# Optimization experiments

Measured on AMD Instinct MI355X. Metric: run time of the kernel, lower is better.

Reference implementation:

```python
import jax, jax.numpy as jnp
import numpy as np
from jax import lax

# FPN anchor layout: 800x800 image, 3 anchors/loc, strides 4,8,16,32,64
LEVEL_ANCHORS = [120000, 30000, 7500, 1875, 507]
PRE_NMS_TOP_N = 1000   # per level (test mode)
POST_NMS_TOP_N = 1000
NMS_THRESH = 0.7
MIN_SIZE = 1e-3


def setup_inputs() -> dict:
    key = jax.random.key(0)
    k1, k2, k3, k4 = jax.random.split(key, 4)
    A = sum(LEVEL_ANCHORS)
    bs = 2
    predicts = jax.random.normal(k1, (bs, A, 4), jnp.float32) * 0.1
    objectness = jax.random.normal(k2, (bs, A, 1), jnp.float32)
    cxy = jax.random.uniform(k3, (A, 2), jnp.float32, 0.0, 800.0)
    wh = jax.random.uniform(k4, (A, 2), jnp.float32, 16.0, 128.0)
    anchors = jnp.concatenate([cxy - 0.5 * wh, cxy + 0.5 * wh], axis=-1)
    valid_size = jnp.full((bs, 2), 800.0, jnp.float32)  # (w, h) per image
    return {"predicts": predicts, "objectness": objectness,
            "anchors": anchors, "valid_size": valid_size}


def _decode(predicts, anchors):
    # BoxCoder.decoder with weights [1,1,1,1]
    awh = anchors[:, 2:] - anchors[:, :2]          # [A,2]
    axy = anchors[:, :2] + 0.5 * awh               # [A,2]
    xy = axy + predicts[..., :2] * awh             # [bs,A,2] center
    wh = jnp.exp(predicts[..., 2:]) * awh          # [bs,A,2]
    x1y1 = xy - 0.5 * wh
    return jnp.concatenate([x1y1, x1y1 + wh], axis=-1)  # [bs,A,4]


def _per_level_topk_idx(scores):
    # scores: [bs, A] -> concat of per-level top-k indices (global anchor ids)
    idx_list, offset = [], 0
    for n in LEVEL_ANCHORS:
        k = min(PRE_NMS_TOP_N, n)
        _, top = lax.top_k(scores[:, offset:offset + n], k)
        idx_list.append(top + offset)
        offset += n
    return jnp.concatenate(idx_list, axis=1)  # [bs, K]


def _nms_keep(boxes, valid, thresh):
    # boxes sorted by score desc; returns boolean keep mask (sequential NMS)
    x1, y1, x2, y2 = boxes[:, 0], boxes[:, 1], boxes[:, 2], boxes[:, 3]
    area = (x2 - x1) * (y2 - y1)
    xx1 = jnp.maximum(x1[:, None], x1[None, :])
    yy1 = jnp.maximum(y1[:, None], y1[None, :])
    xx2 = jnp.minimum(x2[:, None], x2[None, :])
    yy2 = jnp.minimum(y2[:, None], y2[None, :])
    inter = jnp.maximum(xx2 - xx1, 0.0) * jnp.maximum(yy2 - yy1, 0.0)
    iou = inter / (area[:, None] + area[None, :] - inter + 1e-9)
    sup = iou > thresh                                   # [N,N]
    N = boxes.shape[0]
    ar = jnp.arange(N)

    def body(i, keep):
        suppressed = jnp.any((ar < i) & keep & sup[i])
        return keep.at[i].set(keep[i] & ~suppressed)

    return lax.fori_loop(0, N, body, valid)


def _filter_image(boxes, scores, lvls, wh):
    # boxes [K,4], scores [K], lvls [K] int, wh [2]=(w,h)
    w, h = wh[0], wh[1]
    x1 = jnp.clip(boxes[:, 0], 0.0, w)
    y1 = jnp.clip(boxes[:, 1], 0.0, h)
    x2 = jnp.clip(boxes[:, 2], 0.0, w)
    y2 = jnp.clip(boxes[:, 3], 0.0, h)
    boxes = jnp.stack([x1, y1, x2, y2], axis=-1)
    valid = (x2 - x1 > MIN_SIZE) & (y2 - y1 > MIN_SIZE)
    s = jnp.where(valid, scores, -jnp.inf)
    order = jnp.argsort(-s)
    boxes, s, lvls, valid = boxes[order], s[order], lvls[order], valid[order]
    # batched_nms: offset each level into a disjoint coordinate range
    max_coord = lax.stop_gradient(jnp.max(boxes)) + 1.0
    off = lvls.astype(boxes.dtype) * max_coord
    keep = _nms_keep(lax.stop_gradient(boxes) + off[:, None], valid, NMS_THRESH)
    # take first POST_NMS_TOP_N kept (boxes are score-sorted)
    rank = jnp.cumsum(keep) - 1
    slot = jnp.where(keep & (rank < POST_NMS_TOP_N), rank, POST_NMS_TOP_N)
    out_b = jnp.zeros((POST_NMS_TOP_N + 1, 4), boxes.dtype).at[slot].set(boxes)[:POST_NMS_TOP_N]
    out_s = jnp.zeros((POST_NMS_TOP_N + 1,), s.dtype).at[slot].set(
        jnp.where(keep, s, 0.0))[:POST_NMS_TOP_N]
    return out_b, out_s


def reference(predicts, objectness, anchors, valid_size):
    bs = predicts.shape[0]
    proposals = _decode(predicts, anchors)            # [bs,A,4]
    scores = objectness[..., 0]                       # [bs,A]
    idx = _per_level_topk_idx(scores)                 # [bs,K]
    bidx = jnp.arange(bs)[:, None]
    boxes = proposals[bidx, idx]                      # [bs,K,4]
    sc = scores[bidx, idx]                            # [bs,K]
    levels_all = jnp.concatenate(
        [jnp.full((n,), i, jnp.int32) for i, n in enumerate(LEVEL_ANCHORS)])
    lvl = levels_all[idx]                             # [bs,K]
    final_boxes, final_scores = jax.vmap(_filter_image)(boxes, sc, lvl, valid_size)
    return final_boxes, final_scores
```

## Files before the change

### kernel.cpp

```cpp
#include <hip/hip_runtime.h>

typedef unsigned int u32;
typedef unsigned long long u64;

#define A_TOT    159882
#define BS       2
#define KTOP     1000
#define CAND_CAP 4096
#define HB       4096
#define ABLK     4096
#define NBH      40
#define NBLK     (BS * NBH)

static const size_t HIST12_OFF   = 0;
static const size_t CCNT_OFF     = 131072;
static const size_t MAXC_OFF     = 131104;
static const size_t NV_OFF       = 131112;
static const size_t CUTV_OFF     = 131152;
static const size_t BAR_OFF      = 131184;
static const size_t CHUNKANY_OFF = 131264;
static const size_t KEEPS_OFF    = 132544;
static const size_t ZERO_END     = 133824;
static const size_t CAND_OFF     = 133824;
static const size_t LKEY2_OFF    = 395968;
static const size_t LBOX_OFF     = 477888;
static const size_t LSC_OFF      = 641728;
static const size_t RANK_OFF     = 682688;
static const size_t MASK_OFF     = 723648;

__device__ __forceinline__ int level_of(int a) {
  if (a < 120000) return 0;
  if (a < 150000) return 1;
  if (a < 157500) return 2;
  if (a < 159375) return 3;
  return 4;
}

__device__ __forceinline__ u32 dkey(float s) {
  u32 b = __float_as_uint(s);
  return (b & 0x80000000u) ? b : (~b & 0x7FFFFFFFu);
}
__device__ __forceinline__ float dkey_inv(u32 d) {
  u32 b = (d & 0x80000000u) ? d : (~d & 0x7FFFFFFFu);
  return __uint_as_float(b);
}

__device__ __forceinline__ u32 ld_agent_u32(const u32* p) {
  return __hip_atomic_load(p, __ATOMIC_RELAXED, __HIP_MEMORY_SCOPE_AGENT);
}
__device__ __forceinline__ u64 ld_agent_u64(const u64* p) {
  return __hip_atomic_load(p, __ATOMIC_RELAXED, __HIP_MEMORY_SCOPE_AGENT);
}
__device__ __forceinline__ void st_agent_u32(u32* p, u32 v) {
  __hip_atomic_store(p, v, __ATOMIC_RELAXED, __HIP_MEMORY_SCOPE_AGENT);
}
__device__ __forceinline__ void st_agent_u64(u64* p, u64 v) {
  __hip_atomic_store(p, v, __ATOMIC_RELAXED, __HIP_MEMORY_SCOPE_AGENT);
}

__device__ __forceinline__ void gb_arrive(u32* cnt) {
  __syncthreads();
  if (threadIdx.x == 0)
    __hip_atomic_fetch_add(cnt, 1u, __ATOMIC_ACQ_REL, __HIP_MEMORY_SCOPE_AGENT);
}
__device__ __forceinline__ void gb_wait(u32* cnt, u32 nblk) {
  if (threadIdx.x == 0) {
    while (__hip_atomic_load(cnt, __ATOMIC_ACQUIRE, __HIP_MEMORY_SCOPE_AGENT) < nblk)
      __builtin_amdgcn_s_sleep(2);
  }
  __syncthreads();
}

__device__ __forceinline__ void decode_clip(const float* __restrict__ pred,
                                            const float* __restrict__ anch,
                                            const float* __restrict__ vs,
                                            int b, int a,
                                            float& x1c, float& y1c, float& x2c, float& y2c,
                                            bool& valid) {
  const float* pp = pred + ((size_t)b * A_TOT + (size_t)a) * 4;
  const float* aa = anch + (size_t)a * 4;
  float ax1 = aa[0], ay1 = aa[1], ax2 = aa[2], ay2 = aa[3];
  float px = pp[0], py = pp[1], pw = pp[2], ph = pp[3];
  float aw  = __fsub_rn(ax2, ax1);
  float ah  = __fsub_rn(ay2, ay1);
  float acx = __fadd_rn(ax1, __fmul_rn(0.5f, aw));
  float acy = __fadd_rn(ay1, __fmul_rn(0.5f, ah));
  float cx  = __fadd_rn(acx, __fmul_rn(px, aw));
  float cy  = __fadd_rn(acy, __fmul_rn(py, ah));
  float w   = __fmul_rn(expf(pw), aw);
  float h   = __fmul_rn(expf(ph), ah);
  float x1  = __fsub_rn(cx, __fmul_rn(0.5f, w));
  float y1  = __fsub_rn(cy, __fmul_rn(0.5f, h));
  float x2  = __fadd_rn(x1, w);
  float y2  = __fadd_rn(y1, h);
  float Wv = vs[b * 2 + 0], Hv = vs[b * 2 + 1];
  x1c = fminf(fmaxf(x1, 0.0f), Wv);
  y1c = fminf(fmaxf(y1, 0.0f), Hv);
  x2c = fminf(fmaxf(x2, 0.0f), Wv);
  y2c = fminf(fmaxf(y2, 0.0f), Hv);
  valid = (__fsub_rn(x2c, x1c) > 0.001f) && (__fsub_rn(y2c, y1c) > 0.001f);
}

__device__ __forceinline__ void bitonic_u64(u64* arr, int N, int t, int nt) {
  for (int k = 2; k <= N; k <<= 1) {
    for (int j = k >> 1; j > 0; j >>= 1) {
      __syncthreads();
      for (int i = t; i < N; i += nt) {
        int ixj = i ^ j;
        if (ixj > i) {
          u64 x = arr[i], y = arr[ixj];
          bool up = ((i & k) == 0);
          if (up ? (x > y) : (x < y)) { arr[i] = y; arr[ixj] = x; }
        }
      }
    }
  }
  __syncthreads();
}

__device__ __forceinline__ u64 shfl_xor_u64(u64 x, int lanemask) {
  u32 lo = (u32)x, hi = (u32)(x >> 32);
  lo = (u32)__shfl_xor((int)lo, lanemask);
  hi = (u32)__shfl_xor((int)hi, lanemask);
  return ((u64)hi << 32) | (u64)lo;
}

__device__ __forceinline__ u64* regsort2048x(u64 v[2], int tid, u64* bufA, u64* bufB) {
  u64* bufs[2] = {bufA, bufB};
  int cur = 0;
  for (int k = 2; k <= 2048; k <<= 1) {
    for (int j = k >> 1; j > 0; j >>= 1) {
      if (j == 1) {
        bool up = (((2 * tid) & k) == 0);
        u64 a = v[0], b2 = v[1];
        bool sw = up ? (a > b2) : (a < b2);
        if (sw) { v[0] = b2; v[1] = a; }
      } else if (j <= 64) {
        int dl = j >> 1;
        bool up = (((2 * tid) & k) == 0);
        bool low = ((tid & dl) == 0);
        bool keepmin = (low == up);
#pragma unroll
        for (int e = 0; e < 2; ++e) {
          u64 o = shfl_xor_u64(v[e], dl);
          v[e] = keepmin ? (v[e] < o ? v[e] : o) : (v[e] > o ? v[e] : o);
        }
      } else {
        u64* B = bufs[cur]; cur ^= 1;
        B[2 * tid] = v[0]; B[2 * tid + 1] = v[1];
        __syncthreads();
#pragma unroll
        for (int e = 0; e < 2; ++e) {
          int i = 2 * tid + e, p = i ^ j;
          u64 o = B[p];
          bool up = ((i & k) == 0);
          bool keepmin = ((i < p) == up);
          v[e] = keepmin ? (v[e] < o ? v[e] : o) : (v[e] > o ? v[e] : o);
        }
      }
    }
  }
  u64* B = bufs[cur];
  B[2 * tid] = v[0]; B[2 * tid + 1] = v[1];
  __syncthreads();
  return B;
}

__global__ __launch_bounds__(1024)
void k_selsort(const float* __restrict__ pred, const float* __restrict__ obj,
               const float* __restrict__ anch, const float* __restrict__ vs,
               char* __restrict__ ws) {
  __shared__ __align__(16) char smem[82048];
  __shared__ u32 lcnt[2], gbase[2], cutL[2];
  u32* h  = (u32*)smem;
  u32* dk = (u32*)(smem + 32768);
  int tid = threadIdx.x, lane = tid & 63;
  int bid = blockIdx.x;
  int b = bid / NBH, loc = bid % NBH;
  int start = loc * ABLK;
  int l0 = level_of(start);
  bool active = (l0 < 4);
  int nseg = 0;
  u32* barp = (u32*)(ws + BAR_OFF);

  if (active) {
    int lend = level_of(min(start + ABLK - 1, A_TOT - 1));
    nseg = ((l0 + 1 <= lend) && (l0 + 1 < 4)) ? 2 : 1;
    for (int i = tid; i < 2 * HB; i += 1024) h[i] = 0u;
    __syncthreads();
#pragma unroll
    for (int it = 0; it < 4; ++it) {
      int a = start + it * 1024 + tid;
      u32 d = 0;
      if (a < A_TOT) {
        d = dkey(obj[(size_t)b * A_TOT + a]);
        int l = level_of(a);
        if (l < 4) atomicAdd(&h[(u32)(l - l0) * HB + (d >> 20)], 1u);
      }
      dk[it * 1024 + tid] = d;
    }
    __syncthreads();
    for (int s = 0; s < nseg; ++s) {
      u32* gh = (u32*)(ws + HIST12_OFF) + (size_t)(b * 4 + l0 + s) * HB;
      for (int i = tid; i < HB; i += 1024) {
        u32 v = h[s * HB + i];
        if (v) atomicAdd(&gh[i], v);
      }
    }
  }
  gb_arrive(barp + 0); gb_wait(barp + 0, NBLK);

  if (bid < 8) {
    u32* scanS = (u32*)smem;
    const u32* gh = (const u32*)(ws + HIST12_OFF) + (size_t)bid * HB;
    u32 vals[16]; u32 acc = 0;
    if (tid < 256) {
      for (int q = 0; q < 16; ++q) { vals[q] = ld_agent_u32(&gh[tid * 16 + q]); acc += vals[q]; }
      scanS[tid] = acc;
    }
    __syncthreads();
    for (int d = 1; d < 256; d <<= 1) {
      u32 x = (tid < 256 && tid >= d) ? scanS[tid - d] : 0u;
      __syncthreads();
      if (tid < 256) scanS[tid] += x;
      __syncthreads();
    }
    if (tid < 256) {
      u32 incl = scanS[tid], prev = incl - acc;
      if (prev < KTOP && incl >= KTOP) {
        u32 run = prev; int cb = HB - 1;
        for (int q = 0; q < 16; ++q) { run += vals[q]; if (run >= KTOP) { cb = tid * 16 + q; break; } }
        st_agent_u32((u32*)(ws + CUTV_OFF) + bid, (u32)cb);
      }
    }
  }
  gb_arrive(barp + 1); gb_wait(barp + 1, NBLK);

  if (active) {
    if (tid < 2) lcnt[tid] = 0;
    if (tid < nseg) cutL[tid] = ld_agent_u32((const u32*)(ws + CUTV_OFF) + b * 4 + l0 + tid);
    __syncthreads();
    u32 dv[4], slotv[4], passm = 0, sim = 0;
#pragma unroll
    for (int it = 0; it < 4; ++it) {
      int a = start + it * 1024 + tid;
      bool pass = false; u32 si = 0;
      u32 d = dk[it * 1024 + tid];
      if (a < A_TOT) {
        int l = level_of(a);
        if (l < 4) { si = (u32)(l - l0); pass = (d >> 20) <= cutL[si]; }
      }
      dv[it] = d;
      u64 mp = __ballot(pass);
      u64 m1 = __ballot(pass && si == 1);
      u64 m0 = mp & ~m1;
      u32 slot = 0;
      if (m0) {
        int ld = __builtin_ctzll(m0);
        u32 wb = 0;
        if (lane == ld) wb = atomicAdd(&lcnt[0], (u32)__popcll(m0));
        wb = __shfl(wb, ld);
        if (pass && si == 0) slot = wb + (u32)__popcll(m0 & ((1ull << lane) - 1ull));
      }
      if (m1) {
        int ld = __builtin_ctzll(m1);
        u32 wb = 0;
        if (lane == ld) wb = atomicAdd(&lcnt[1], (u32)__popcll(m1));
        wb = __shfl(wb, ld);
        if (pass && si == 1) slot = wb + (u32)__popcll(m1 & ((1ull << lane) - 1ull));
      }
      slotv[it] = slot;
      if (pass) { passm |= 1u << it; if (si) sim |= 1u << it; }
    }
    __syncthreads();
    if (tid < 2)
      gbase[tid] = lcnt[tid] ? atomicAdd((u32*)(ws + CCNT_OFF) + (b * 4 + l0 + tid), lcnt[tid]) : 0u;
    __syncthreads();
#pragma unroll
    for (int it = 0; it < 4; ++it) {
      if ((passm >> it) & 1u) {
        int a = start + it * 1024 + tid;
        u32 si = (sim >> it) & 1u;
        int seg = b * 4 + l0 + (int)si;
        u32 gslot = gbase[si] + slotv[it];
        if (gslot < CAND_CAP)
          st_agent_u64((u64*)(ws + CAND_OFF) + (size_t)seg * CAND_CAP + gslot,
                       ((u64)dv[it] << 32) | ((u64)(u32)a << 12) | (u64)gslot);
      }
    }
  }
  gb_arrive(barp + 2);
  if (bid >= 10) return;
  gb_wait(barp + 2, NBLK);

  u64*    bufAB  = (u64*)smem;
  float4* dboxS  = (float4*)(smem + 32768);
  float*  dscS   = (float*)(smem + 65536);
  u32*    validS = (u32*)(smem + 73728);
  u64*    cm     = (u64*)(smem + 81920);
  u64* bufA = bufAB; u64* bufB = bufAB + 2048;
  int wv = tid >> 6;
  int P = bid, l = P % 5;
  b = P / 5;
  int n;
  u64* S;
  if (l == 4) {
    n = 507;
    u64 v[2];
#pragma unroll
    for (int e = 0; e < 2; ++e) {
      int idx = 2 * tid + e;
      if (idx < 507) {
        int a = 159375 + idx;
        float sc = obj[(size_t)b * A_TOT + a];
        float x1, y1, x2, y2; bool valid;
        decode_clip(pred, anch, vs, b, a, x1, y1, x2, y2, valid);
        dboxS[idx] = make_float4(x1, y1, x2, y2);
        dscS[idx] = sc;
        validS[idx] = valid ? 1u : 0u;
        v[e] = ((u64)dkey(sc) << 32) | ((u64)(u32)a << 12) | (u64)idx;
      } else v[e] = ~0ull;
    }
    S = regsort2048x(v, tid, bufA, bufB);
  } else {
    n = KTOP;
    int seg = b * 4 + l;
    u32 cnt = min(ld_agent_u32((const u32*)(ws + CCNT_OFF) + seg), (u32)CAND_CAP);
    const u64* cand = (const u64*)(ws + CAND_OFF) + (size_t)seg * CAND_CAP;
    if (cnt <= 2048) {
      u64 v[2];
#pragma unroll
      for (int e = 0; e < 2; ++e) {
        int idx = 2 * tid + e;
        if (idx < (int)cnt) {
          u64 key = ld_agent_u64(&cand[idx]);
          int a = (int)((key >> 12) & 0x3FFFFu);
          float x1, y1, x2, y2; bool valid;
          decode_clip(pred, anch, vs, b, a, x1, y1, x2, y2, valid);
          dboxS[idx] = make_float4(x1, y1, x2, y2);
          dscS[idx] = dkey_inv((u32)(key >> 32));
          validS[idx] = valid ? 1u : 0u;
          v[e] = key;
        } else v[e] = ~0ull;
      }
      S = regsort2048x(v, tid, bufA, bufB);
    } else {
      int N = 2048; while (N < (int)cnt) N <<= 1;
      for (int i = tid; i < N; i += 1024)
        bufAB[i] = (i < (int)cnt) ? ld_agent_u64(&cand[i]) : ~0ull;
      bitonic_u64(bufAB, N, tid, 1024);
      for (int j = tid; j < KTOP; j += 1024) {
        u64 key = bufAB[j];
        int a = (int)((key >> 12) & 0x3FFFFu);
        float x1, y1, x2, y2; bool valid;
        decode_clip(pred, anch, vs, b, a, x1, y1, x2, y2, valid);
        dboxS[j] = make_float4(x1, y1, x2, y2);
        dscS[j] = dkey_inv((u32)(key >> 32));
        validS[j] = valid ? 1u : 0u;
        bufAB[j] = (key & ~0xFFFull) | (u64)j;
      }
      __syncthreads();
      S = bufAB;
    }
  }
  float m = 0.0f;
  for (int j = tid; j < n; j += 1024) {
    int slot = (int)(S[j] & 0xFFFull);
    float4 bx = dboxS[slot];
    m = fmaxf(m, fmaxf(fmaxf(bx.x, bx.y), fmaxf(bx.z, bx.w)));
  }
  for (int off = 32; off; off >>= 1) m = fmaxf(m, __shfl_xor(m, off));
  if (lane == 0) atomicMax((u32*)(ws + MAXC_OFF) + b, __float_as_uint(m));
  {
    int j = wv * 64 + lane;
    bool val = (j < n) && (validS[(int)(S[j] & 0xFFFull)] != 0u);
    u64 mask = __ballot(val);
    if (lane == 0) cm[wv] = mask;
    __syncthreads();
    int base = 0;
    for (int w2 = 0; w2 < wv; ++w2) base += __popcll(cm[w2]);
    if (val) {
      int r = base + __popcll(mask & ((1ull << lane) - 1ull));
      int slot = (int)(S[j] & 0xFFFull);
      ((u64*)(ws + LKEY2_OFF))[(size_t)P * 1024 + r] = S[j];
      ((float4*)(ws + LBOX_OFF))[(size_t)P * 1024 + r] = dboxS[slot];
      ((float*)(ws + LSC_OFF))[(size_t)P * 1024 + r] = dscS[slot];
    }
    if (tid == 0) {
      int tot = 0;
      for (int w2 = 0; w2 < 16; ++w2) tot += __popcll(cm[w2]);
      ((u32*)(ws + NV_OFF))[P] = (u32)tot;
    }
  }
}

__global__ __launch_bounds__(1024)
void k_nms(float* __restrict__ out, char* __restrict__ ws) {
  __shared__ __align__(16) char smem[130304];
  float4* boxS  = (float4*)smem;
  float*  areaS = (float*)(smem + 16384);
  u64*    maskL = (u64*)smem;
  u64* keepsF = (u64*)(smem + 128000);
  u64* kbF    = (u64*)(smem + 128640);
  u32* sbF    = (u32*)(smem + 129280);
  u32* pfxF   = (u32*)(smem + 129792);
  u32* nvsF   = (u32*)(smem + 130112);
  int tid = threadIdx.x, lane = tid & 63;
  int bid = blockIdx.x;
  int P = bid >> 4, rseg = bid & 15;
  int b = P / 5, l = P % 5;
  u32* barp = (u32*)(ws + BAR_OFF);
  int n = (int)((const u32*)(ws + NV_OFF))[P];
  int W = (n + 63) >> 6;
  {
    float M = __uint_as_float(((const u32*)(ws + MAXC_OFF))[b]);
    float off = __fmul_rn((float)l, __fadd_rn(M, 1.0f));
    const float4* lbox = (const float4*)(ws + LBOX_OFF) + (size_t)P * 1024;
    for (int i = tid; i < n; i += 1024) {
      float4 bx = lbox[i];
      bx.x = __fadd_rn(bx.x, off); bx.y = __fadd_rn(bx.y, off);
      bx.z = __fadd_rn(bx.z, off); bx.w = __fadd_rn(bx.w, off);
      boxS[i] = bx;
      areaS[i] = __fmul_rn(__fsub_rn(bx.z, bx.x), __fsub_rn(bx.w, bx.y));
    }
    if (tid < 64) {
      int e = rseg * 64 + tid;
      if (e < n) {
        const u64* lkey = (const u64*)(ws + LKEY2_OFF);
        const u32* nvp = (const u32*)(ws + NV_OFF);
        u64 key = lkey[(size_t)P * 1024 + e];
        const u64* base[4];
        int lo[4], hi[4], q2 = 0;
        for (int l2 = 0; l2 < 5; ++l2) {
          if (l2 == l) continue;
          base[q2] = lkey + (size_t)(b * 5 + l2) * 1024;
          lo[q2] = 0; hi[q2] = (int)nvp[b * 5 + l2];
          ++q2;
        }
        for (int step = 0; step < 11; ++step) {
#pragma unroll
          for (int q = 0; q < 4; ++q) {
            if (lo[q] < hi[q]) {
              int mid = (lo[q] + hi[q]) >> 1;
              u64 v = base[q][mid];
              if (v < key) lo[q] = mid + 1; else hi[q] = mid;
            }
          }
        }
        st_agent_u32((u32*)(ws + RANK_OFF) + (size_t)P * 1024 + e,
                     (u32)(e + lo[0] + lo[1] + lo[2] + lo[3]));
      }
    }
    __syncthreads();
    int i = rseg * 64 + (tid >> 4);
    int w = tid & 15;
    if (i < n && w < W && w >= rseg) {
      float4 bi = boxS[i];
      float ai = areaS[i];
      u64 word = 0;
      int j0 = w << 6;
      int jn = min(64, n - j0);
      if (jn == 64) {
#pragma unroll 4
        for (int t2 = 0; t2 < 64; ++t2) {
          int jj = (t2 + w) & 63;
          float4 bj = boxS[j0 + jj];
          float xx1 = fmaxf(bi.x, bj.x);
          float yy1 = fmaxf(bi.y, bj.y);
          float xx2 = fminf(bi.z, bj.z);
          float yy2 = fminf(bi.w, bj.w);
          float iw = fmaxf(__fsub_rn(xx2, xx1), 0.0f);
          float ih = fmaxf(__fsub_rn(yy2, yy1), 0.0f);
          float inter = __fmul_rn(iw, ih);
          float den = __fadd_rn(__fsub_rn(__fadd_rn(ai, areaS[j0 + jj]), inter), 1e-9f);
          float iou = __fdiv_rn(inter, den);
          if (iou > 0.7f) word |= (1ull << jj);
        }
      } else {
        for (int jj = 0; jj < jn; ++jj) {
          float4 bj = boxS[j0 + jj];
          float xx1 = fmaxf(bi.x, bj.x);
          float yy1 = fmaxf(bi.y, bj.y);
          float xx2 = fminf(bi.z, bj.z);
          float yy2 = fminf(bi.w, bj.w);
          float iw = fmaxf(__fsub_rn(xx2, xx1), 0.0f);
          float ih = fmaxf(__fsub_rn(yy2, yy1), 0.0f);
          float inter = __fmul_rn(iw, ih);
          float den = __fadd_rn(__fsub_rn(__fadd_rn(ai, areaS[j0 + jj]), inter), 1e-9f);
          float iou = __fdiv_rn(inter, den);
          if (iou > 0.7f) word |= (1ull << jj);
        }
      }
      if (w == rseg) word &= ~(1ull << (i & 63));
      st_agent_u64((u64*)(ws + MASK_OFF) + (size_t)P * 16000 + (size_t)i * W + w, word);
      if (word)
        atomicOr((u64*)(ws + CHUNKANY_OFF) + (size_t)P * 16 + (i >> 6), 1ull << (i & 63));
    }
  }
  gb_arrive(barp + 3);
  if (rseg != 0) return;
  gb_wait(barp + 3, 160);

  {
    const u64* maskg = (const u64*)(ws + MASK_OFF) + (size_t)P * 16000;
    int T = n * W;
    for (int t = tid; t < T; t += 1024) maskL[t] = ld_agent_u64(&maskg[t]);
    __syncthreads();
    if (tid < 64) {
      u64 ca = (lane < 16) ? ld_agent_u64((const u64*)(ws + CHUNKANY_OFF) + (size_t)P * 16 + lane)
                           : 0ull;
      u64 dpre[16];
#pragma unroll
      for (int c = 0; c < 16; ++c) {
        int row = (c << 6) + lane;
        dpre[c] = (c < W && row < n) ? maskL[(size_t)row * W + c] : 0ull;
      }
      u64 removed = 0ull, keepw = 0ull;
#pragma unroll
      for (int c = 0; c < 16; ++c) {
        if (c >= W) break;
        int rb = c << 6;
        int rows = min(64, n - rb);
        u64 rowsmask = (rows == 64) ? ~0ull : ((1ull << rows) - 1ull);
        u64 curw = __shfl(removed, c);
        u64 cand = ~curw & rowsmask;
        u64 ca_c = __shfl(ca, c);
        u64 keptbits;
        u64 anyrows = ca_c & cand;
        if (anyrows == 0ull) {
          keptbits = cand;
        } else {
          u64 diag = dpre[c];
          u64 diagnz = __ballot(diag != 0ull) & cand;
          if (diagnz == 0ull) {
            keptbits = cand;
          } else {
            u64 remw = curw | ~rowsmask;
            u64 kept = 0ull;
            int pos = 0;
            u64 work = diagnz;
            while (work) {
              int s = __builtin_ctzll(work); work &= work - 1;
              u64 range = (1ull << s) - (1ull << pos);
              kept |= ~remw & range;
              bool k = ((remw >> s) & 1ull) == 0ull;
              u64 dr = __shfl(diag, s);
              if (k) { kept |= 1ull << s; remw |= dr; }
              pos = s + 1;
            }
            u64 tail = (pos >= 64) ? 0ull : (~0ull << pos);
            kept |= ~remw & tail & rowsmask;
            keptbits = kept;
          }
          u64 todo = keptbits & ca_c;
          while (todo) {
            int r0 = __builtin_ctzll(todo); todo &= todo - 1;
            int r1 = -1, r2 = -1, r3 = -1;
            if (todo) { r1 = __builtin_ctzll(todo); todo &= todo - 1; }
            if (todo) { r2 = __builtin_ctzll(todo); todo &= todo - 1; }
            if (todo) { r3 = __builtin_ctzll(todo); todo &= todo - 1; }
            u64 v0 = 0, v1 = 0, v2 = 0, v3 = 0;
            if (lane < W) {
              v0 = maskL[(size_t)(rb + r0) * W + lane];
              if (r1 >= 0) v1 = maskL[(size_t)(rb + r1) * W + lane];
              if (r2 >= 0) v2 = maskL[(size_t)(rb + r2) * W + lane];
              if (r3 >= 0) v3 = maskL[(size_t)(rb + r3) * W + lane];
            }
            removed |= v0 | v1 | v2 | v3;
          }
        }
        if (lane == c) keepw |= keptbits;
      }
      if (lane < 16)
        st_agent_u64((u64*)(ws + KEEPS_OFF) + (size_t)P * 16 + lane, keepw);
    }
  }
  gb_arrive(barp + 4);
  if (l != 0) return;
  gb_wait(barp + 4, 10);

  for (int i = tid; i < 80; i += 1024) {
    keepsF[i] = ld_agent_u64((const u64*)(ws + KEEPS_OFF) + (size_t)b * 80 + i);
    kbF[i] = 0ull;
  }
  if (tid < 5) nvsF[tid] = ((const u32*)(ws + NV_OFF))[b * 5 + tid];
  for (int i = tid; i < 4000; i += 1024) out[(size_t)b * 4000 + i] = 0.0f;
  for (int i = tid; i < 1000; i += 1024) out[8000 + (size_t)b * 1000 + i] = 0.0f;
  __syncthreads();
  const u32* rank = (const u32*)(ws + RANK_OFF);
  for (int idx = tid; idx < 5120; idx += 1024) {
    int p = idx >> 10, i = idx & 1023;
    if (i < (int)nvsF[p] && ((keepsF[p * 16 + (i >> 6)] >> (i & 63)) & 1ull)) {
      u32 r = ld_agent_u32(&rank[(size_t)(b * 5 + p) * 1024 + i]);
      atomicOr(&kbF[r >> 6], 1ull << (r & 63));
    }
  }
  __syncthreads();
  if (tid < 128) sbF[tid] = (tid < 80) ? (u32)__popcll(kbF[tid]) : 0u;
  __syncthreads();
  for (int d = 1; d < 128; d <<= 1) {
    u32 x = (tid < 128 && tid >= d) ? sbF[tid - d] : 0u;
    __syncthreads();
    if (tid < 128) sbF[tid] += x;
    __syncthreads();
  }
  if (tid < 80) pfxF[tid] = sbF[tid] - (u32)__popcll(kbF[tid]);
  __syncthreads();
  for (int idx = tid; idx < 5120; idx += 1024) {
    int p = idx >> 10, i = idx & 1023;
    if (i < (int)nvsF[p] && ((keepsF[p * 16 + (i >> 6)] >> (i & 63)) & 1ull)) {
      int Pp = b * 5 + p;
      u32 r = ld_agent_u32(&rank[(size_t)Pp * 1024 + i]);
      u64 word = kbF[r >> 6];
      int slot = (int)pfxF[r >> 6] + __popcll(word & ((1ull << (r & 63)) - 1ull));
      if (slot < KTOP) {
        float4 bx = ((const float4*)(ws + LBOX_OFF))[(size_t)Pp * 1024 + i];
        float s = ((const float*)(ws + LSC_OFF))[(size_t)Pp * 1024 + i];
        float* ob = out + ((size_t)b * KTOP + slot) * 4;
        ob[0] = bx.x; ob[1] = bx.y; ob[2] = bx.z; ob[3] = bx.w;
        out[8000 + (size_t)b * KTOP + slot] = s;
      }
    }
  }
}

extern "C" void kernel_launch(void* const* d_in, const int* in_sizes, int n_in,
                              void* d_out, int out_size, void* d_ws, size_t ws_size,
                              hipStream_t stream) {
  const float* pred = (const float*)d_in[0];
  const float* obj  = (const float*)d_in[1];
  const float* anch = (const float*)d_in[2];
  const float* vs   = (const float*)d_in[3];
  float* out = (float*)d_out;
  char* ws = (char*)d_ws;
  (void)in_sizes; (void)n_in; (void)out_size; (void)ws_size;

  hipMemsetAsync(ws, 0, ZERO_END, stream);
  k_selsort<<<NBLK, 1024, 0, stream>>>(pred, obj, anch, vs, ws);
  k_nms    <<<160,  1024, 0, stream>>>(out, ws);
}
```

Before: 167.0 us.

## Fuse selection and NMS kernels into one with per-segment dataflow flags

Merges the two kernels into a single 160-block kernel. The grid-wide barriers are replaced by per-segment and per-image counters, so each stage waits only on its actual producers: histogram contributors, compaction, sort per image, mask rows per partition. Each block now computes its own cutoff scan, removing a barrier, and the cross-level binary search reads keys staged in shared memory. The cost is more shared memory per block, and correctness now depends on all 160 blocks being resident at once, since they spin-wait on each other.

Measured after the change: 196.6 us. 17.7% more time.

```diff
diff --git a/kernel.cpp b/kernel.cpp
--- a/kernel.cpp
+++ b/kernel.cpp
@@ -10,23 +10,25 @@
 #define HB       4096
 #define ABLK     4096
 #define NBH      40
-#define NBLK     (BS * NBH)
 
 static const size_t HIST12_OFF   = 0;
 static const size_t CCNT_OFF     = 131072;
 static const size_t MAXC_OFF     = 131104;
 static const size_t NV_OFF       = 131112;
-static const size_t CUTV_OFF     = 131152;
-static const size_t BAR_OFF      = 131184;
-static const size_t CHUNKANY_OFF = 131264;
-static const size_t KEEPS_OFF    = 132544;
-static const size_t ZERO_END     = 133824;
-static const size_t CAND_OFF     = 133824;
-static const size_t LKEY2_OFF    = 395968;
-static const size_t LBOX_OFF     = 477888;
-static const size_t LSC_OFF      = 641728;
-static const size_t RANK_OFF     = 682688;
-static const size_t MASK_OFF     = 723648;
+static const size_t F_HIST_OFF   = 131152;
+static const size_t F_COMP_OFF   = 131184;
+static const size_t F_SD_OFF     = 131216;
+static const size_t F_MASK_OFF   = 131224;
+static const size_t F_SCAN_OFF   = 131264;
+static const size_t CHUNKANY_OFF = 131328;
+static const size_t KEEPS_OFF    = 132608;
+static const size_t ZERO_END     = 133888;
+static const size_t CAND_OFF     = 133888;
+static const size_t LKEY2_OFF    = 396032;
+static const size_t LBOX_OFF     = 477952;
+static const size_t LSC_OFF      = 641792;
+static const size_t RANK_OFF     = 682752;
+static const size_t MASK_OFF     = 723712;
 
 __device__ __forceinline__ int level_of(int a) {
   if (a < 120000) return 0;
@@ -35,6 +37,9 @@
   if (a < 159375) return 3;
   return 4;
 }
+__device__ __forceinline__ u32 ncontrib(int l) {
+  return l == 0 ? 30u : (l == 1 ? 8u : (l == 2 ? 3u : 1u));
+}
 
 __device__ __forceinline__ u32 dkey(float s) {
   u32 b = __float_as_uint(s);
@@ -57,15 +62,26 @@
 __device__ __forceinline__ void st_agent_u64(u64* p, u64 v) {
   __hip_atomic_store(p, v, __ATOMIC_RELAXED, __HIP_MEMORY_SCOPE_AGENT);
 }
-
-__device__ __forceinline__ void gb_arrive(u32* cnt) {
+__device__ __forceinline__ void st_agent_f4(float4* p, float4 v) {
+  union { float4 f; u64 q[2]; } u; u.f = v;
+  u64* d = (u64*)p;
+  st_agent_u64(d, u.q[0]); st_agent_u64(d + 1, u.q[1]);
+}
+__device__ __forceinline__ float4 ld_agent_f4(const float4* p) {
+  union { float4 f; u64 q[2]; } u;
+  const u64* s = (const u64*)p;
+  u.q[0] = ld_agent_u64(s); u.q[1] = ld_agent_u64(s + 1);
+  return u.f;
+}
+
+__device__ __forceinline__ void flag_bump(u32* f) {
   __syncthreads();
   if (threadIdx.x == 0)
-    __hip_atomic_fetch_add(cnt, 1u, __ATOMIC_ACQ_REL, __HIP_MEMORY_SCOPE_AGENT);
-}
-__device__ __forceinline__ void gb_wait(u32* cnt, u32 nblk) {
+    __hip_atomic_fetch_add(f, 1u, __ATOMIC_ACQ_REL, __HIP_MEMORY_SCOPE_AGENT);
+}
+__device__ __forceinline__ void flag_wait(u32* f, u32 tgt) {
   if (threadIdx.x == 0) {
-    while (__hip_atomic_load(cnt, __ATOMIC_ACQUIRE, __HIP_MEMORY_SCOPE_AGENT) < nblk)
+    while (__hip_atomic_load(f, __ATOMIC_ACQUIRE, __HIP_MEMORY_SCOPE_AGENT) < tgt)
       __builtin_amdgcn_s_sleep(2);
   }
   __syncthreads();
@@ -167,282 +183,288 @@
 }
 
 __global__ __launch_bounds__(1024)
-void k_selsort(const float* __restrict__ pred, const float* __restrict__ obj,
-               const float* __restrict__ anch, const float* __restrict__ vs,
-               char* __restrict__ ws) {
-  __shared__ __align__(16) char smem[82048];
+void k_mega(const float* __restrict__ pred, const float* __restrict__ obj,
+            const float* __restrict__ anch, const float* __restrict__ vs,
+            float* __restrict__ out, char* __restrict__ ws) {
+  __shared__ __align__(16) char smem[130816];
   __shared__ u32 lcnt[2], gbase[2], cutL[2];
-  u32* h  = (u32*)smem;
-  u32* dk = (u32*)(smem + 32768);
   int tid = threadIdx.x, lane = tid & 63;
   int bid = blockIdx.x;
-  int b = bid / NBH, loc = bid % NBH;
-  int start = loc * ABLK;
-  int l0 = level_of(start);
-  bool active = (l0 < 4);
-  int nseg = 0;
-  u32* barp = (u32*)(ws + BAR_OFF);
-
-  if (active) {
-    int lend = level_of(min(start + ABLK - 1, A_TOT - 1));
-    nseg = ((l0 + 1 <= lend) && (l0 + 1 < 4)) ? 2 : 1;
-    for (int i = tid; i < 2 * HB; i += 1024) h[i] = 0u;
-    __syncthreads();
-#pragma unroll
-    for (int it = 0; it < 4; ++it) {
-      int a = start + it * 1024 + tid;
-      u32 d = 0;
-      if (a < A_TOT) {
-        d = dkey(obj[(size_t)b * A_TOT + a]);
-        int l = level_of(a);
-        if (l < 4) atomicAdd(&h[(u32)(l - l0) * HB + (d >> 20)], 1u);
-      }
-      dk[it * 1024 + tid] = d;
-    }
-    __syncthreads();
-    for (int s = 0; s < nseg; ++s) {
-      u32* gh = (u32*)(ws + HIST12_OFF) + (size_t)(b * 4 + l0 + s) * HB;
-      for (int i = tid; i < HB; i += 1024) {
-        u32 v = h[s * HB + i];
-        if (v) atomicAdd(&gh[i], v);
-      }
-    }
-  }
-  gb_arrive(barp + 0); gb_wait(barp + 0, NBLK);
-
-  if (bid < 8) {
-    u32* scanS = (u32*)smem;
-    const u32* gh = (const u32*)(ws + HIST12_OFF) + (size_t)bid * HB;
-    u32 vals[16]; u32 acc = 0;
-    if (tid < 256) {
-      for (int q = 0; q < 16; ++q) { vals[q] = ld_agent_u32(&gh[tid * 16 + q]); acc += vals[q]; }
-      scanS[tid] = acc;
-    }
-    __syncthreads();
-    for (int d = 1; d < 256; d <<= 1) {
-      u32 x = (tid < 256 && tid >= d) ? scanS[tid - d] : 0u;
-      __syncthreads();
-      if (tid < 256) scanS[tid] += x;
-      __syncthreads();
-    }
-    if (tid < 256) {
-      u32 incl = scanS[tid], prev = incl - acc;
-      if (prev < KTOP && incl >= KTOP) {
-        u32 run = prev; int cb = HB - 1;
-        for (int q = 0; q < 16; ++q) { run += vals[q]; if (run >= KTOP) { cb = tid * 16 + q; break; } }
-        st_agent_u32((u32*)(ws + CUTV_OFF) + bid, (u32)cb);
-      }
-    }
-  }
-  gb_arrive(barp + 1); gb_wait(barp + 1, NBLK);
-
-  if (active) {
-    if (tid < 2) lcnt[tid] = 0;
-    if (tid < nseg) cutL[tid] = ld_agent_u32((const u32*)(ws + CUTV_OFF) + b * 4 + l0 + tid);
-    __syncthreads();
-    u32 dv[4], slotv[4], passm = 0, sim = 0;
-#pragma unroll
-    for (int it = 0; it < 4; ++it) {
-      int a = start + it * 1024 + tid;
-      bool pass = false; u32 si = 0;
-      u32 d = dk[it * 1024 + tid];
-      if (a < A_TOT) {
-        int l = level_of(a);
-        if (l < 4) { si = (u32)(l - l0); pass = (d >> 20) <= cutL[si]; }
-      }
-      dv[it] = d;
-      u64 mp = __ballot(pass);
-      u64 m1 = __ballot(pass && si == 1);
-      u64 m0 = mp & ~m1;
-      u32 slot = 0;
-      if (m0) {
-        int ld = __builtin_ctzll(m0);
-        u32 wb = 0;
-        if (lane == ld) wb = atomicAdd(&lcnt[0], (u32)__popcll(m0));
-        wb = __shfl(wb, ld);
-        if (pass && si == 0) slot = wb + (u32)__popcll(m0 & ((1ull << lane) - 1ull));
-      }
-      if (m1) {
-        int ld = __builtin_ctzll(m1);
-        u32 wb = 0;
-        if (lane == ld) wb = atomicAdd(&lcnt[1], (u32)__popcll(m1));
-        wb = __shfl(wb, ld);
-        if (pass && si == 1) slot = wb + (u32)__popcll(m1 & ((1ull << lane) - 1ull));
-      }
-      slotv[it] = slot;
-      if (pass) { passm |= 1u << it; if (si) sim |= 1u << it; }
-    }
-    __syncthreads();
-    if (tid < 2)
-      gbase[tid] = lcnt[tid] ? atomicAdd((u32*)(ws + CCNT_OFF) + (b * 4 + l0 + tid), lcnt[tid]) : 0u;
-    __syncthreads();
-#pragma unroll
-    for (int it = 0; it < 4; ++it) {
-      if ((passm >> it) & 1u) {
+  u32* FH = (u32*)(ws + F_HIST_OFF);
+  u32* FC = (u32*)(ws + F_COMP_OFF);
+  u32* FS = (u32*)(ws + F_SD_OFF);
+  u32* FM = (u32*)(ws + F_MASK_OFF);
+  u32* FN = (u32*)(ws + F_SCAN_OFF);
+
+  if (bid < 80) {
+    int b = bid / NBH, loc = bid % NBH;
+    int start = loc * ABLK;
+    int l0 = level_of(start);
+    if (l0 < 4) {
+      u32* h  = (u32*)smem;
+      u32* dk = (u32*)(smem + 32768);
+      int lend = level_of(min(start + ABLK - 1, A_TOT - 1));
+      int nseg = ((l0 + 1 <= lend) && (l0 + 1 < 4)) ? 2 : 1;
+      for (int i = tid; i < 2 * HB; i += 1024) h[i] = 0u;
+      __syncthreads();
+#pragma unroll
+      for (int it = 0; it < 4; ++it) {
         int a = start + it * 1024 + tid;
-        u32 si = (sim >> it) & 1u;
-        int seg = b * 4 + l0 + (int)si;
-        u32 gslot = gbase[si] + slotv[it];
-        if (gslot < CAND_CAP)
-          st_agent_u64((u64*)(ws + CAND_OFF) + (size_t)seg * CAND_CAP + gslot,
-                       ((u64)dv[it] << 32) | ((u64)(u32)a << 12) | (u64)gslot);
-      }
-    }
-  }
-  gb_arrive(barp + 2);
-  if (bid >= 10) return;
-  gb_wait(barp + 2, NBLK);
-
-  u64*    bufAB  = (u64*)smem;
-  float4* dboxS  = (float4*)(smem + 32768);
-  float*  dscS   = (float*)(smem + 65536);
-  u32*    validS = (u32*)(smem + 73728);
-  u64*    cm     = (u64*)(smem + 81920);
-  u64* bufA = bufAB; u64* bufB = bufAB + 2048;
-  int wv = tid >> 6;
-  int P = bid, l = P % 5;
-  b = P / 5;
-  int n;
-  u64* S;
-  if (l == 4) {
-    n = 507;
-    u64 v[2];
-#pragma unroll
-    for (int e = 0; e < 2; ++e) {
-      int idx = 2 * tid + e;
-      if (idx < 507) {
-        int a = 159375 + idx;
-        float sc = obj[(size_t)b * A_TOT + a];
-        float x1, y1, x2, y2; bool valid;
-        decode_clip(pred, anch, vs, b, a, x1, y1, x2, y2, valid);
-        dboxS[idx] = make_float4(x1, y1, x2, y2);
-        dscS[idx] = sc;
-        validS[idx] = valid ? 1u : 0u;
-        v[e] = ((u64)dkey(sc) << 32) | ((u64)(u32)a << 12) | (u64)idx;
-      } else v[e] = ~0ull;
-    }
-    S = regsort2048x(v, tid, bufA, bufB);
-  } else {
-    n = KTOP;
-    int seg = b * 4 + l;
-    u32 cnt = min(ld_agent_u32((const u32*)(ws + CCNT_OFF) + seg), (u32)CAND_CAP);
-    const u64* cand = (const u64*)(ws + CAND_OFF) + (size_t)seg * CAND_CAP;
-    if (cnt <= 2048) {
+        u32 d = 0;
+        if (a < A_TOT) {
+          d = dkey(obj[(size_t)b * A_TOT + a]);
+          int l = level_of(a);
+          if (l < 4) atomicAdd(&h[(u32)(l - l0) * HB + (d >> 20)], 1u);
+        }
+        dk[it * 1024 + tid] = d;
+      }
+      __syncthreads();
+      for (int s = 0; s < nseg; ++s) {
+        u32* gh = (u32*)(ws + HIST12_OFF) + (size_t)(b * 4 + l0 + s) * HB;
+        for (int i = tid; i < HB; i += 1024) {
+          u32 v = h[s * HB + i];
+          if (v) atomicAdd(&gh[i], v);
+        }
+      }
+      __syncthreads();
+      if (tid == 0)
+        for (int s = 0; s < nseg; ++s)
+          __hip_atomic_fetch_add(FH + b * 4 + l0 + s, 1u, __ATOMIC_ACQ_REL,
+                                 __HIP_MEMORY_SCOPE_AGENT);
+      for (int s = 0; s < nseg; ++s)
+        flag_wait(FH + b * 4 + l0 + s, ncontrib(l0 + s));
+      u32* scanS = (u32*)(smem + 49152);
+      for (int s = 0; s < nseg; ++s) {
+        int seg = b * 4 + l0 + s;
+        const u32* gh = (const u32*)(ws + HIST12_OFF) + (size_t)seg * HB;
+        u32 vals[16]; u32 acc = 0;
+        if (tid < 256) {
+          for (int q = 0; q < 16; ++q) { vals[q] = ld_agent_u32(&gh[tid * 16 + q]); acc += vals[q]; }
+          scanS[tid] = acc;
+        }
+        __syncthreads();
+        for (int d = 1; d < 256; d <<= 1) {
+          u32 x = (tid < 256 && tid >= d) ? scanS[tid - d] : 0u;
+          __syncthreads();
+          if (tid < 256) scanS[tid] += x;
+          __syncthreads();
+        }
+        if (tid < 256) {
+          u32 incl = scanS[tid], prev = incl - acc;
+          if (prev < KTOP && incl >= KTOP) {
+            u32 run = prev; int cb = HB - 1;
+            for (int q = 0; q < 16; ++q) { run += vals[q]; if (run >= KTOP) { cb = tid * 16 + q; break; } }
+            cutL[s] = (u32)cb;
+          }
+        }
+        __syncthreads();
+      }
+      if (tid < 2) lcnt[tid] = 0;
+      __syncthreads();
+      u32 dv[4], slotv[4], passm = 0, sim = 0;
+#pragma unroll
+      for (int it = 0; it < 4; ++it) {
+        int a = start + it * 1024 + tid;
+        bool pass = false; u32 si = 0;
+        u32 d = dk[it * 1024 + tid];
+        if (a < A_TOT) {
+          int l = level_of(a);
+          if (l < 4) { si = (u32)(l - l0); pass = (d >> 20) <= cutL[si]; }
+        }
+        dv[it] = d;
+        u64 mp = __ballot(pass);
+        u64 m1 = __ballot(pass && si == 1);
+        u64 m0 = mp & ~m1;
+        u32 slot = 0;
+        if (m0) {
+          int ld = __builtin_ctzll(m0);
+          u32 wb = 0;
+          if (lane == ld) wb = atomicAdd(&lcnt[0], (u32)__popcll(m0));
+          wb = __shfl(wb, ld);
+          if (pass && si == 0) slot = wb + (u32)__popcll(m0 & ((1ull << lane) - 1ull));
+        }
+        if (m1) {
+          int ld = __builtin_ctzll(m1);
+          u32 wb = 0;
+          if (lane == ld) wb = atomicAdd(&lcnt[1], (u32)__popcll(m1));
+          wb = __shfl(wb, ld);
+          if (pass && si == 1) slot = wb + (u32)__popcll(m1 & ((1ull << lane) - 1ull));
+        }
+        slotv[it] = slot;
+        if (pass) { passm |= 1u << it; if (si) sim |= 1u << it; }
+      }
+      __syncthreads();
+      if (tid < 2)
+        gbase[tid] = lcnt[tid] ? atomicAdd((u32*)(ws + CCNT_OFF) + (b * 4 + l0 + tid), lcnt[tid]) : 0u;
+      __syncthreads();
+#pragma unroll
+      for (int it = 0; it < 4; ++it) {
+        if ((passm >> it) & 1u) {
+          int a = start + it * 1024 + tid;
+          u32 si = (sim >> it) & 1u;
+          int seg = b * 4 + l0 + (int)si;
+          u32 gslot = gbase[si] + slotv[it];
+          if (gslot < CAND_CAP)
+            st_agent_u64((u64*)(ws + CAND_OFF) + (size_t)seg * CAND_CAP + gslot,
+                         ((u64)dv[it] << 32) | ((u64)(u32)a << 12) | (u64)gslot);
+        }
+      }
+      __syncthreads();
+      if (tid == 0)
+        for (int s = 0; s < nseg; ++s)
+          __hip_atomic_fetch_add(FC + b * 4 + l0 + s, 1u, __ATOMIC_ACQ_REL,
+                                 __HIP_MEMORY_SCOPE_AGENT);
+    }
+  }
+
+  if (bid < 10) {
+    u64*    bufAB  = (u64*)smem;
+    float4* dboxS  = (float4*)(smem + 32768);
+    float*  dscS   = (float*)(smem + 65536);
+    u32*    validS = (u32*)(smem + 73728);
+    u64*    cm     = (u64*)(smem + 81920);
+    u64* bufA = bufAB; u64* bufB = bufAB + 2048;
+    int wv = tid >> 6;
+    int P = bid, b = P / 5, l = P % 5;
+    if (l < 4) flag_wait(FC + b * 4 + l, ncontrib(l));
+    else __syncthreads();
+    int n;
+    u64* S;
+    if (l == 4) {
+      n = 507;
       u64 v[2];
 #pragma unroll
       for (int e = 0; e < 2; ++e) {
         int idx = 2 * tid + e;
-        if (idx < (int)cnt) {
-          u64 key = ld_agent_u64(&cand[idx]);
+        if (idx < 507) {
+          int a = 159375 + idx;
+          float sc = obj[(size_t)b * A_TOT + a];
+          float x1, y1, x2, y2; bool valid;
+          decode_clip(pred, anch, vs, b, a, x1, y1, x2, y2, valid);
+          dboxS[idx] = make_float4(x1, y1, x2, y2);
+          dscS[idx] = sc;
+          validS[idx] = valid ? 1u : 0u;
+          v[e] = ((u64)dkey(sc) << 32) | ((u64)(u32)a << 12) | (u64)idx;
+        } else v[e] = ~0ull;
+      }
+      S = regsort2048x(v, tid, bufA, bufB);
+    } else {
+      n = KTOP;
+      int seg = b * 4 + l;
+      u32 cnt = min(ld_agent_u32((const u32*)(ws + CCNT_OFF) + seg), (u32)CAND_CAP);
+      const u64* cand = (const u64*)(ws + CAND_OFF) + (size_t)seg * CAND_CAP;
+      if (cnt <= 2048) {
+        u64 v[2];
+#pragma unroll
+        for (int e = 0; e < 2; ++e) {
+          int idx = 2 * tid + e;
+          if (idx < (int)cnt) {
+            u64 key = ld_agent_u64(&cand[idx]);
+            int a = (int)((key >> 12) & 0x3FFFFu);
+            float x1, y1, x2, y2; bool valid;
+            decode_clip(pred, anch, vs, b, a, x1, y1, x2, y2, valid);
+            dboxS[idx] = make_float4(x1, y1, x2, y2);
+            dscS[idx] = dkey_inv((u32)(key >> 32));
+            validS[idx] = valid ? 1u : 0u;
+            v[e] = key;
+          } else v[e] = ~0ull;
+        }
+        S = regsort2048x(v, tid, bufA, bufB);
+      } else {
+        int N = 2048; while (N < (int)cnt) N <<= 1;
+        for (int i = tid; i < N; i += 1024)
+          bufAB[i] = (i < (int)cnt) ? ld_agent_u64(&cand[i]) : ~0ull;
+        bitonic_u64(bufAB, N, tid, 1024);
+        for (int j = tid; j < KTOP; j += 1024) {
+          u64 key = bufAB[j];
           int a = (int)((key >> 12) & 0x3FFFFu);
           float x1, y1, x2, y2; bool valid;
           decode_clip(pred, anch, vs, b, a, x1, y1, x2, y2, valid);
-          dboxS[idx] = make_float4(x1, y1, x2, y2);
-          dscS[idx] = dkey_inv((u32)(key >> 32));
-          validS[idx] = valid ? 1u : 0u;
-          v[e] = key;
-        } else v[e] = ~0ull;
-      }
-      S = regsort2048x(v, tid, bufA, bufB);
-    } else {
-      int N = 2048; while (N < (int)cnt) N <<= 1;
-      for (int i = tid; i < N; i += 1024)
-        bufAB[i] = (i < (int)cnt) ? ld_agent_u64(&cand[i]) : ~0ull;
-      bitonic_u64(bufAB, N, tid, 1024);
-      for (int j = tid; j < KTOP; j += 1024) {
-        u64 key = bufAB[j];
-        int a = (int)((key >> 12) & 0x3FFFFu);
-        float x1, y1, x2, y2; bool valid;
-        decode_clip(pred, anch, vs, b, a, x1, y1, x2, y2, valid);
-        dboxS[j] = make_float4(x1, y1, x2, y2);
-        dscS[j] = dkey_inv((u32)(key >> 32));
-        validS[j] = valid ? 1u : 0u;
-        bufAB[j] = (key & ~0xFFFull) | (u64)j;
-      }
-      __syncthreads();
-      S = bufAB;
-    }
-  }
-  float m = 0.0f;
-  for (int j = tid; j < n; j += 1024) {
-    int slot = (int)(S[j] & 0xFFFull);
-    float4 bx = dboxS[slot];
-    m = fmaxf(m, fmaxf(fmaxf(bx.x, bx.y), fmaxf(bx.z, bx.w)));
-  }
-  for (int off = 32; off; off >>= 1) m = fmaxf(m, __shfl_xor(m, off));
-  if (lane == 0) atomicMax((u32*)(ws + MAXC_OFF) + b, __float_as_uint(m));
-  {
-    int j = wv * 64 + lane;
-    bool val = (j < n) && (validS[(int)(S[j] & 0xFFFull)] != 0u);
-    u64 mask = __ballot(val);
-    if (lane == 0) cm[wv] = mask;
-    __syncthreads();
-    int base = 0;
-    for (int w2 = 0; w2 < wv; ++w2) base += __popcll(cm[w2]);
-    if (val) {
-      int r = base + __popcll(mask & ((1ull << lane) - 1ull));
+          dboxS[j] = make_float4(x1, y1, x2, y2);
+          dscS[j] = dkey_inv((u32)(key >> 32));
+          validS[j] = valid ? 1u : 0u;
+          bufAB[j] = (key & ~0xFFFull) | (u64)j;
+        }
+        __syncthreads();
+        S = bufAB;
+      }
+    }
+    float m = 0.0f;
+    for (int j = tid; j < n; j += 1024) {
       int slot = (int)(S[j] & 0xFFFull);
-      ((u64*)(ws + LKEY2_OFF))[(size_t)P * 1024 + r] = S[j];
-      ((float4*)(ws + LBOX_OFF))[(size_t)P * 1024 + r] = dboxS[slot];
-      ((float*)(ws + LSC_OFF))[(size_t)P * 1024 + r] = dscS[slot];
-    }
-    if (tid == 0) {
-      int tot = 0;
-      for (int w2 = 0; w2 < 16; ++w2) tot += __popcll(cm[w2]);
-      ((u32*)(ws + NV_OFF))[P] = (u32)tot;
-    }
-  }
-}
-
-__global__ __launch_bounds__(1024)
-void k_nms(float* __restrict__ out, char* __restrict__ ws) {
-  __shared__ __align__(16) char smem[130304];
-  float4* boxS  = (float4*)smem;
-  float*  areaS = (float*)(smem + 16384);
-  u64*    maskL = (u64*)smem;
-  u64* keepsF = (u64*)(smem + 128000);
-  u64* kbF    = (u64*)(smem + 128640);
-  u32* sbF    = (u32*)(smem + 129280);
-  u32* pfxF   = (u32*)(smem + 129792);
-  u32* nvsF   = (u32*)(smem + 130112);
-  int tid = threadIdx.x, lane = tid & 63;
-  int bid = blockIdx.x;
+      float4 bx = dboxS[slot];
+      m = fmaxf(m, fmaxf(fmaxf(bx.x, bx.y), fmaxf(bx.z, bx.w)));
+    }
+    for (int off = 32; off; off >>= 1) m = fmaxf(m, __shfl_xor(m, off));
+    if (lane == 0) atomicMax((u32*)(ws + MAXC_OFF) + b, __float_as_uint(m));
+    {
+      int j = wv * 64 + lane;
+      bool val = (j < n) && (validS[(int)(S[j] & 0xFFFull)] != 0u);
+      u64 mask = __ballot(val);
+      if (lane == 0) cm[wv] = mask;
+      __syncthreads();
+      int base = 0;
+      for (int w2 = 0; w2 < wv; ++w2) base += __popcll(cm[w2]);
+      if (val) {
+        int r = base + __popcll(mask & ((1ull << lane) - 1ull));
+        int slot = (int)(S[j] & 0xFFFull);
+        st_agent_u64((u64*)(ws + LKEY2_OFF) + (size_t)P * 1024 + r, S[j]);
+        st_agent_f4((float4*)(ws + LBOX_OFF) + (size_t)P * 1024 + r, dboxS[slot]);
+        st_agent_u32((u32*)(ws + LSC_OFF) + (size_t)P * 1024 + r,
+                     __float_as_uint(dscS[slot]));
+      }
+      if (tid == 0) {
+        int tot = 0;
+        for (int w2 = 0; w2 < 16; ++w2) tot += __popcll(cm[w2]);
+        st_agent_u32((u32*)(ws + NV_OFF) + P, (u32)tot);
+      }
+    }
+    flag_bump(FS + b);
+  }
+
   int P = bid >> 4, rseg = bid & 15;
-  int b = P / 5, l = P % 5;
-  u32* barp = (u32*)(ws + BAR_OFF);
-  int n = (int)((const u32*)(ws + NV_OFF))[P];
+  int mb = P / 5, ml = P % 5;
+  flag_wait(FS + mb, 5);
+  int n = (int)ld_agent_u32((const u32*)(ws + NV_OFF) + P);
   int W = (n + 63) >> 6;
   {
-    float M = __uint_as_float(((const u32*)(ws + MAXC_OFF))[b]);
-    float off = __fmul_rn((float)l, __fadd_rn(M, 1.0f));
+    float4* boxS  = (float4*)smem;
+    float*  areaS = (float*)(smem + 16384);
+    u64*    lkeyS = (u64*)(smem + 20480);
+    u32*    nvO   = (u32*)(smem + 53248);
+    float M = __uint_as_float(ld_agent_u32((const u32*)(ws + MAXC_OFF) + mb));
+    float off = __fmul_rn((float)ml, __fadd_rn(M, 1.0f));
     const float4* lbox = (const float4*)(ws + LBOX_OFF) + (size_t)P * 1024;
     for (int i = tid; i < n; i += 1024) {
-      float4 bx = lbox[i];
+      float4 bx = ld_agent_f4(&lbox[i]);
       bx.x = __fadd_rn(bx.x, off); bx.y = __fadd_rn(bx.y, off);
       bx.z = __fadd_rn(bx.z, off); bx.w = __fadd_rn(bx.w, off);
       boxS[i] = bx;
       areaS[i] = __fmul_rn(__fsub_rn(bx.z, bx.x), __fsub_rn(bx.w, bx.y));
     }
+    if (tid < 4) {
+      int l2 = tid + (tid >= ml ? 1 : 0);
+      nvO[tid] = ld_agent_u32((const u32*)(ws + NV_OFF) + mb * 5 + l2);
+    }
+    for (int t = tid; t < 4096; t += 1024) {
+      int q = t >> 10, i = t & 1023;
+      int l2 = q + (q >= ml ? 1 : 0);
+      lkeyS[t] = ld_agent_u64((const u64*)(ws + LKEY2_OFF) + (size_t)(mb * 5 + l2) * 1024 + i);
+    }
+    __syncthreads();
     if (tid < 64) {
       int e = rseg * 64 + tid;
       if (e < n) {
-        const u64* lkey = (const u64*)(ws + LKEY2_OFF);
-        const u32* nvp = (const u32*)(ws + NV_OFF);
-        u64 key = lkey[(size_t)P * 1024 + e];
-        const u64* base[4];
-        int lo[4], hi[4], q2 = 0;
-        for (int l2 = 0; l2 < 5; ++l2) {
-          if (l2 == l) continue;
-          base[q2] = lkey + (size_t)(b * 5 + l2) * 1024;
-          lo[q2] = 0; hi[q2] = (int)nvp[b * 5 + l2];
-          ++q2;
-        }
+        u64 key = ld_agent_u64((const u64*)(ws + LKEY2_OFF) + (size_t)P * 1024 + e);
+        int lo[4], hi[4];
+#pragma unroll
+        for (int q = 0; q < 4; ++q) { lo[q] = 0; hi[q] = (int)nvO[q]; }
         for (int step = 0; step < 11; ++step) {
 #pragma unroll
           for (int q = 0; q < 4; ++q) {
             if (lo[q] < hi[q]) {
               int mid = (lo[q] + hi[q]) >> 1;
-              u64 v = base[q][mid];
+              u64 v = lkeyS[q * 1024 + mid];
               if (v < key) lo[q] = mid + 1; else hi[q] = mid;
             }
           }
@@ -497,18 +519,20 @@
         atomicOr((u64*)(ws + CHUNKANY_OFF) + (size_t)P * 16 + (i >> 6), 1ull << (i & 63));
     }
   }
-  gb_arrive(barp + 3);
-  if (rseg != 0) return;
-  gb_wait(barp + 3, 160);
-
+  flag_bump(FM + P);
+  if (rseg != 15) return;
+
+  flag_wait(FM + P, 16);
   {
+    u64* maskL = (u64*)smem;
     const u64* maskg = (const u64*)(ws + MASK_OFF) + (size_t)P * 16000;
     int T = n * W;
     for (int t = tid; t < T; t += 1024) maskL[t] = ld_agent_u64(&maskg[t]);
     __syncthreads();
     if (tid < 64) {
-      u64 ca = (lane < 16) ? ld_agent_u64((const u64*)(ws + CHUNKANY_OFF) + (size_t)P * 16 + lane)
-                           : 0ull;
+      u64 ca = (lane < 16)
+                 ? ld_agent_u64((const u64*)(ws + CHUNKANY_OFF) + (size_t)P * 16 + lane)
+                 : 0ull;
       u64 dpre[16];
 #pragma unroll
       for (int c = 0; c < 16; ++c) {
@@ -575,50 +599,58 @@
         st_agent_u64((u64*)(ws + KEEPS_OFF) + (size_t)P * 16 + lane, keepw);
     }
   }
-  gb_arrive(barp + 4);
-  if (l != 0) return;
-  gb_wait(barp + 4, 10);
-
-  for (int i = tid; i < 80; i += 1024) {
-    keepsF[i] = ld_agent_u64((const u64*)(ws + KEEPS_OFF) + (size_t)b * 80 + i);
-    kbF[i] = 0ull;
-  }
-  if (tid < 5) nvsF[tid] = ((const u32*)(ws + NV_OFF))[b * 5 + tid];
-  for (int i = tid; i < 4000; i += 1024) out[(size_t)b * 4000 + i] = 0.0f;
-  for (int i = tid; i < 1000; i += 1024) out[8000 + (size_t)b * 1000 + i] = 0.0f;
-  __syncthreads();
-  const u32* rank = (const u32*)(ws + RANK_OFF);
-  for (int idx = tid; idx < 5120; idx += 1024) {
-    int p = idx >> 10, i = idx & 1023;
-    if (i < (int)nvsF[p] && ((keepsF[p * 16 + (i >> 6)] >> (i & 63)) & 1ull)) {
-      u32 r = ld_agent_u32(&rank[(size_t)(b * 5 + p) * 1024 + i]);
-      atomicOr(&kbF[r >> 6], 1ull << (r & 63));
-    }
-  }
-  __syncthreads();
-  if (tid < 128) sbF[tid] = (tid < 80) ? (u32)__popcll(kbF[tid]) : 0u;
-  __syncthreads();
-  for (int d = 1; d < 128; d <<= 1) {
-    u32 x = (tid < 128 && tid >= d) ? sbF[tid - d] : 0u;
+  flag_bump(FN + mb);
+  if (ml != 0) return;
+
+  flag_wait(FN + mb, 5);
+  {
+    u64* keepsF = (u64*)(smem + 128000);
+    u64* kbF    = (u64*)(smem + 128640);
+    u32* sbF    = (u32*)(smem + 129280);
+    u32* pfxF   = (u32*)(smem + 129792);
+    u32* nvsF   = (u32*)(smem + 130112);
+    int b = mb;
+    for (int i = tid; i < 80; i += 1024) {
+      keepsF[i] = ld_agent_u64((const u64*)(ws + KEEPS_OFF) + (size_t)b * 80 + i);
+      kbF[i] = 0ull;
+    }
+    if (tid < 5) nvsF[tid] = ld_agent_u32((const u32*)(ws + NV_OFF) + b * 5 + tid);
+    for (int i = tid; i < 4000; i += 1024) out[(size_t)b * 4000 + i] = 0.0f;
+    for (int i = tid; i < 1000; i += 1024) out[8000 + (size_t)b * 1000 + i] = 0.0f;
     __syncthreads();
-    if (tid < 128) sbF[tid] += x;
+    const u32* rank = (const u32*)(ws + RANK_OFF);
+    for (int idx = tid; idx < 5120; idx += 1024) {
+      int p = idx >> 10, i = idx & 1023;
+      if (i < (int)nvsF[p] && ((keepsF[p * 16 + (i >> 6)] >> (i & 63)) & 1ull)) {
+        u32 r = ld_agent_u32(&rank[(size_t)(b * 5 + p) * 1024 + i]);
+        atomicOr(&kbF[r >> 6], 1ull << (r & 63));
+      }
+    }
     __syncthreads();
-  }
-  if (tid < 80) pfxF[tid] = sbF[tid] - (u32)__popcll(kbF[tid]);
-  __syncthreads();
-  for (int idx = tid; idx < 5120; idx += 1024) {
-    int p = idx >> 10, i = idx & 1023;
-    if (i < (int)nvsF[p] && ((keepsF[p * 16 + (i >> 6)] >> (i & 63)) & 1ull)) {
-      int Pp = b * 5 + p;
-      u32 r = ld_agent_u32(&rank[(size_t)Pp * 1024 + i]);
-      u64 word = kbF[r >> 6];
-      int slot = (int)pfxF[r >> 6] + __popcll(word & ((1ull << (r & 63)) - 1ull));
-      if (slot < KTOP) {
-        float4 bx = ((const float4*)(ws + LBOX_OFF))[(size_t)Pp * 1024 + i];
-        float s = ((const float*)(ws + LSC_OFF))[(size_t)Pp * 1024 + i];
-        float* ob = out + ((size_t)b * KTOP + slot) * 4;
-        ob[0] = bx.x; ob[1] = bx.y; ob[2] = bx.z; ob[3] = bx.w;
-        out[8000 + (size_t)b * KTOP + slot] = s;
+    if (tid < 128) sbF[tid] = (tid < 80) ? (u32)__popcll(kbF[tid]) : 0u;
+    __syncthreads();
+    for (int d = 1; d < 128; d <<= 1) {
+      u32 x = (tid < 128 && tid >= d) ? sbF[tid - d] : 0u;
+      __syncthreads();
+      if (tid < 128) sbF[tid] += x;
+      __syncthreads();
+    }
+    if (tid < 80) pfxF[tid] = sbF[tid] - (u32)__popcll(kbF[tid]);
+    __syncthreads();
+    for (int idx = tid; idx < 5120; idx += 1024) {
+      int p = idx >> 10, i = idx & 1023;
+      if (i < (int)nvsF[p] && ((keepsF[p * 16 + (i >> 6)] >> (i & 63)) & 1ull)) {
+        int Pp = b * 5 + p;
+        u32 r = ld_agent_u32(&rank[(size_t)Pp * 1024 + i]);
+        u64 word = kbF[r >> 6];
+        int slot = (int)pfxF[r >> 6] + __popcll(word & ((1ull << (r & 63)) - 1ull));
+        if (slot < KTOP) {
+          float4 bx = ld_agent_f4((const float4*)(ws + LBOX_OFF) + (size_t)Pp * 1024 + i);
+          float s = __uint_as_float(ld_agent_u32((const u32*)(ws + LSC_OFF) + (size_t)Pp * 1024 + i));
+          float* ob = out + ((size_t)b * KTOP + slot) * 4;
+          ob[0] = bx.x; ob[1] = bx.y; ob[2] = bx.z; ob[3] = bx.w;
+          out[8000 + (size_t)b * KTOP + slot] = s;
+        }
       }
     }
   }
@@ -636,6 +668,5 @@
   (void)in_sizes; (void)n_in; (void)out_size; (void)ws_size;
 
   hipMemsetAsync(ws, 0, ZERO_END, stream);
-  k_selsort<<<NBLK, 1024, 0, stream>>>(pred, obj, anch, vs, ws);
-  k_nms    <<<160,  1024, 0, stream>>>(out, ws);
-}
+  k_mega<<<160, 1024, 0, stream>>>(pred, obj, anch, vs, out, ws);
+}
```
